# Kernel optimization log

Hardware: AMD Instinct MI355X
Metric: run time of the kernel (lower is better)

## Reference

```python
import jax, jax.numpy as jnp
import numpy as np

N_PHY = 12
NMUL = 4
WARM_UP = 365
NEARZERO = 1e-5
LENF = 15

# parameter_bounds order: BETA, FC, K0, K1, K2, LP, PERC, UZL, TT, CFMAX, CFR, CWH
PHY_LB = jnp.array([1.0, 50.0, 0.05, 0.01, 0.001, 0.2, 0.0, 0.0, -2.5, 0.5, 0.0, 0.0], dtype=jnp.float32)
PHY_UB = jnp.array([6.0, 1000.0, 0.9, 0.5, 0.2, 1.0, 10.0, 100.0, 2.5, 10.0, 0.1, 0.2], dtype=jnp.float32)
ROUTE_A_LB, ROUTE_A_UB = 0.0, 2.9
ROUTE_B_LB, ROUTE_B_UB = 0.0, 6.5


def _hbv_scan(p, t, pet, states, phy):
    """Run HBV step recurrence over time. p/t/pet: [T,G]; states: 5-tuple of [G,M]."""
    beta, fc, k0, k1, k2, lp, perc, uzl, tt, cfmax, cfr, cwh = phy  # each [G,M]

    def step(carry, xt):
        snowpack, meltwater, sm, suz, slz = carry
        Pt, Tt, PETt = xt
        Pt, Tt, PETt = Pt[:, None], Tt[:, None], PETt[:, None]  # [G,1] bcast vs [G,M]
        is_rain = (Tt >= tt).astype(sm.dtype)
        rain = Pt * is_rain
        snow = Pt * (1.0 - is_rain)
        snowpack = snowpack + snow
        melt = jnp.minimum(jnp.maximum(cfmax * (Tt - tt), 0.0), snowpack)
        meltwater = meltwater + melt
        snowpack = snowpack - melt
        refreeze = jnp.minimum(jnp.maximum(cfr * cfmax * (tt - Tt), 0.0), meltwater)
        snowpack = snowpack + refreeze
        meltwater = meltwater - refreeze
        tosoil = jnp.maximum(meltwater - cwh * snowpack, 0.0)
        meltwater = meltwater - tosoil
        soil_wetness = jnp.clip((sm / fc) ** beta, 0.0, 1.0)
        recharge = (rain + tosoil) * soil_wetness
        sm = sm + rain + tosoil - recharge
        excess = jnp.maximum(sm - fc, 0.0)
        sm = sm - excess
        evapfactor = jnp.clip(sm / (lp * fc), 0.0, 1.0)
        etact = jnp.minimum(sm, PETt * evapfactor)
        sm = jnp.maximum(sm - etact, NEARZERO)
        suz = suz + recharge + excess
        prc = jnp.minimum(suz, perc)
        suz = suz - prc
        q0 = k0 * jnp.maximum(suz - uzl, 0.0)
        suz = suz - q0
        q1 = k1 * suz
        suz = suz - q1
        slz = slz + prc
        q2 = k2 * slz
        slz = slz - q2
        return (snowpack, meltwater, sm, suz, slz), q0 + q1 + q2

    states, qs = jax.lax.scan(step, states, (p, t, pet))
    return qs, states  # qs: [T,G,M]


def _forward(x_phy, parameters):
    T, G, _ = x_phy.shape
    p, t, pet = x_phy[..., 0], x_phy[..., 1], x_phy[..., 2]
    # unpack physical params from last param timestep, map [0,1] -> bounds
    raw = parameters[-1, :, : N_PHY * NMUL].reshape(G, N_PHY, NMUL)
    phy_all = PHY_LB[None, :, None] + raw * (PHY_UB - PHY_LB)[None, :, None]
    phy = tuple(phy_all[:, i, :] for i in range(N_PHY))  # (beta, fc, k0, k1, k2, lp, perc, uzl, tt, cfmax, cfr, cwh)
    route = parameters[-1, :, N_PHY * NMUL :]
    a = ROUTE_A_LB + route[:, 0] * (ROUTE_A_UB - ROUTE_A_LB)
    b = ROUTE_B_LB + route[:, 1] * (ROUTE_B_UB - ROUTE_B_LB)

    s0 = jnp.full((G, NMUL), 0.001, dtype=x_phy.dtype)
    states = (s0, s0, s0, s0, s0)

    # warm-up under stop_gradient (matches torch.no_grad in original)
    phy_ng = jax.tree_util.tree_map(jax.lax.stop_gradient, phy)
    q_warm, states = _hbv_scan(
        jax.lax.stop_gradient(p[:WARM_UP]),
        jax.lax.stop_gradient(t[:WARM_UP]),
        jax.lax.stop_gradient(pet[:WARM_UP]),
        states, phy_ng)
    states = jax.tree_util.tree_map(jax.lax.stop_gradient, states)
    q_warm = jax.lax.stop_gradient(q_warm)

    q_pred, _ = _hbv_scan(p[WARM_UP:], t[WARM_UP:], pet[WARM_UP:], states, phy)
    qs = jnp.concatenate([q_warm, q_pred], axis=0).mean(-1)  # [T,G]

    # gamma unit hydrograph weights, [LENF, G]
    tg = (jnp.arange(LENF, dtype=qs.dtype) + 0.5)[:, None]
    aa = jax.nn.relu(a)[None, :] + 0.1
    th = jax.nn.relu(b)[None, :] + 0.5
    w = (tg ** (aa - 1.0)) * jnp.exp(-tg / th) / (jnp.exp(jax.scipy.special.gammaln(aa)) * th ** aa)
    w = w / w.sum(0)

    # causal depthwise (per-basin) convolution along time
    conv = jax.vmap(lambda q, u: jnp.convolve(q, u)[:T])(qs.T, w.T)  # [G,T]
    streamflow = conv.T[:, :, None]  # [T,G,1]
    return streamflow[WARM_UP:]


def setup_inputs() -> dict:
    key = jax.random.key(0)
    k1, k2, k3, k4 = jax.random.split(key, 4)
    T, G = 2000, 4000
    prcp = jax.random.uniform(k1, (T, G), dtype=jnp.float32) * 10.0   # mm/day
    tmean = jax.random.normal(k2, (T, G), dtype=jnp.float32) * 8.0    # degC
    pet = jax.random.uniform(k3, (T, G), dtype=jnp.float32) * 5.0     # mm/day
    x_phy = jnp.stack([prcp, tmean, pet], axis=-1)
    parameters = jax.random.uniform(k4, (1, G, N_PHY * NMUL + 2), dtype=jnp.float32)
    return {"x_phy": x_phy, "parameters": parameters}


def reference(x_phy, parameters):
    return _forward(x_phy, parameters)
```

## Files before the change

kernel.cpp:

```cpp
#include <hip/hip_runtime.h>

#define TT    2000
#define NG    4000
#define WARM  365
#define LENF  15
#define NPHY  12
#define BLK   60
#define PAIRS (BLK / 2)
#define SLOTW 64
#define SLOTD (BLK * SLOTW)
#define NBLK  34
#define ROWF  (3 * NG)

typedef const float __attribute__((address_space(1)))* gptr_t;
typedef float __attribute__((address_space(3)))* lptr_t;
typedef __attribute__((ext_vector_type(2))) float f32x2;

__device__ __forceinline__ float quad_sum(float x) {
    int a = __builtin_amdgcn_update_dpp(0, __float_as_int(x), 0xB1, 0xF, 0xF, true);
    float s = x + __int_as_float(a);
    int b = __builtin_amdgcn_update_dpp(0, __float_as_int(s), 0x4E, 0xF, 0xF, true);
    return s + __int_as_float(b);
}

#define WG_BARRIER() asm volatile("s_waitcnt lgkmcnt(0)\n\ts_barrier" ::: "memory")

__global__ __launch_bounds__(256, 1) void hbv_pipe_kernel(
    const float* __restrict__ xphy,
    const float* __restrict__ prm,
    float* __restrict__ out)
{
    __shared__ float s_stage[3 * SLOTD];
    __shared__ f32x2 s_rt [2 * PAIRS * 64];
    __shared__ f32x2 s_rex[2 * PAIRS * 64];
    __shared__ f32x2 s_q  [2 * PAIRS * 64];

    const int lane = threadIdx.x & 63;
    const int wid  = threadIdx.x >> 6;
    const int g0   = blockIdx.x * 16;
    const int cell = lane >> 2;
    const int g    = g0 + cell;
    const int m    = lane & 3;

    const float* pg = prm + (size_t)g * (NPHY * 4 + 2);

    const float lb[NPHY] = {1.0f, 50.0f, 0.05f, 0.01f, 0.001f, 0.2f, 0.0f, 0.0f, -2.5f, 0.5f, 0.0f, 0.0f};
    const float ub[NPHY] = {6.0f, 1000.0f, 0.9f, 0.5f, 0.2f, 1.0f, 10.0f, 100.0f, 2.5f, 10.0f, 0.1f, 0.2f};
    float ph[NPHY];
    #pragma unroll
    for (int i = 0; i < NPHY; ++i)
        ph[i] = lb[i] + pg[i * 4 + m] * (ub[i] - lb[i]);

    const float beta = ph[0], fc = ph[1], k0 = ph[2], k1 = ph[3], k2 = ph[4],
                lp = ph[5], perc = ph[6], uzl = ph[7], ttp = ph[8],
                cfmax = ph[9], cfr = ph[10], cwh = ph[11];
    const float rfc    = 1.0f / fc;
    const float rlpfc  = 1.0f / (lp * fc);
    const float cfrcf  = cfr * cfmax;
    const float blfc   = beta * __builtin_amdgcn_logf(rfc);
    const float onemk1 = 1.0f - k1;
    const float onemk2 = 1.0f - k2;

    const float aa  = fmaxf(pg[48] * 2.9f, 0.0f) + 0.1f;
    const float th  = fmaxf(pg[49] * 6.5f, 0.0f) + 0.5f;
    const float rth = 1.0f / th;
    const float LOG2E = 1.4426950408889634f;
    float w[LENF];
    float wsum = 0.0f;
    #pragma unroll
    for (int k = 0; k < LENF; ++k) {
        const float tg = (float)k + 0.5f;
        const float e = (aa - 1.0f) * __builtin_log2f(tg) - tg * rth * LOG2E;
        w[k] = __builtin_amdgcn_exp2f(e);
        wsum += w[k];
    }
    const float rw = 0.25f / wsum;
    #pragma unroll
    for (int k = 0; k < LENF; ++k) w[k] *= rw;

    float snowpack = 0.001f, meltwater = 0.001f;
    float sm = 0.001f;
    float suz = 0.001f, slz = 0.001f;
    float qh[BLK + LENF - 1];
    #pragma unroll
    for (int d = 0; d < BLK + LENF - 1; ++d) qh[d] = 0.0f;

    const int loffd = (lane < 48 ? lane : 47);
    const float* ga = xphy + (size_t)(wid * 15) * ROWF + g0 * 3 + loffd;

    {
        float* ldst = &s_stage[(wid * 15) * SLOTW];
        #pragma unroll
        for (int cc = 0; cc < 15; ++cc) {
            __builtin_amdgcn_global_load_lds((gptr_t)ga, (lptr_t)(ldst + cc * SLOTW), 4, 0, 0);
            ga += ROWF;
        }
        ga += 45 * ROWF;
    }
    asm volatile("s_waitcnt vmcnt(0)" ::: "memory");
    WG_BARRIER();

    for (int i = 0; i <= NBLK + 2; ++i) {
        if (i < NBLK - 1) {
            const int sl = (i + 1) % 3;
            float* ldst = &s_stage[sl * SLOTD + (wid * 15) * SLOTW];
            if (i + 1 == NBLK - 1) {
                #pragma unroll
                for (int cc = 0; cc < 15; ++cc) {
                    int t = (NBLK - 1) * BLK + wid * 15 + cc;
                    if (t > TT - 1) t = TT - 1;
                    const float* gsrc = xphy + (size_t)t * ROWF + g0 * 3 + loffd;
                    __builtin_amdgcn_global_load_lds((gptr_t)gsrc, (lptr_t)(ldst + cc * SLOTW), 4, 0, 0);
                }
            } else {
                const float* gp2 = ga;
                #pragma unroll
                for (int cc = 0; cc < 15; ++cc) {
                    __builtin_amdgcn_global_load_lds((gptr_t)gp2, (lptr_t)(ldst + cc * SLOTW), 4, 0, 0);
                    gp2 += ROWF;
                }
                ga = gp2 + 45 * ROWF;
            }
        }

        if (wid == 0) {
            if (i < NBLK) {
                const float* sb = &s_stage[(i % 3) * SLOTD + cell * 3];
                f32x2* rtw = &s_rt[(i & 1) * (PAIRS * 64) + lane];
                float rt_even = 0.0f;
                #pragma unroll
                for (int j = 0; j < BLK; ++j) {
                    const float Pt = sb[j * SLOTW];
                    const float Tm = sb[j * SLOTW + 1];
                    const float dT      = Tm - ttp;
                    const float rain    = (Tm >= ttp) ? Pt : 0.0f;
                    const float snow    = Pt - rain;
                    const float meltcap = cfmax * fmaxf(dT, 0.0f);
                    const float refcap  = cfrcf * fmaxf(-dT, 0.0f);
                    snowpack += snow;
                    const float melt = fminf(meltcap, snowpack);
                    meltwater += melt;
                    snowpack  -= melt;
                    const float refreeze = fminf(refcap, meltwater);
                    meltwater -= refreeze;
                    snowpack  += refreeze;
                    const float tosoil = fmaxf(fmaf(-cwh, snowpack, meltwater), 0.0f);
                    meltwater -= tosoil;
                    const float rt = rain + tosoil;
                    if ((j & 1) == 0) rt_even = rt;
                    else {
                        f32x2 pr; pr[0] = rt_even; pr[1] = rt;
                        rtw[(j >> 1) * 64] = pr;
                    }
                }
            }
        } else if (wid == 1) {
            const int b = i - 1;
            if (b >= 0 && b < NBLK) {
                const float* sb = &s_stage[(b % 3) * SLOTD + cell * 3 + 2];
                const f32x2* rtr = &s_rt[(b & 1) * (PAIRS * 64) + lane];
                f32x2* rexw = &s_rex[(b & 1) * (PAIRS * 64) + lane];
                f32x2 prt; prt[0] = 0.0f; prt[1] = 0.0f;
                float rex_even = 0.0f;
                #pragma unroll
                for (int j = 0; j < BLK; ++j) {
                    if ((j & 1) == 0) prt = rtr[(j >> 1) * 64];
                    const float rt = ((j & 1) == 0) ? prt[0] : prt[1];
                    const float ev = sb[j * SLOTW];
                    const float sw    = __builtin_amdgcn_exp2f(fmaf(beta, __builtin_amdgcn_logf(sm), blfc));
                    const float smprt = sm + rt;
                    const float sm1   = fmaf(-rt, sw, smprt);
                    const float sm2   = fminf(sm1, fc);
                    const float uf    = fmaxf(fmaf(-ev, rlpfc, 1.0f), 0.0f);
                    const float av    = sm2 * uf;
                    const float cv    = sm2 - ev;
                    sm = fmaxf(fmaxf(av, cv), 1e-5f);
                    const float rex = fmaf(rt, sw, sm1 - sm2);
                    if ((j & 1) == 0) rex_even = rex;
                    else {
                        f32x2 pr; pr[0] = rex_even; pr[1] = rex;
                        rexw[(j >> 1) * 64] = pr;
                    }
                }
            }
        } else if (wid == 2) {
            const int b = i - 2;
            if (b >= 0 && b < NBLK) {
                const f32x2* rexr = &s_rex[(b & 1) * (PAIRS * 64) + lane];
                f32x2* qw = &s_q[(b & 1) * (PAIRS * 64) + lane];
                f32x2 prx; prx[0] = 0.0f; prx[1] = 0.0f;
                float q_even = 0.0f;
                #pragma unroll
                for (int j = 0; j < BLK; ++j) {
                    if ((j & 1) == 0) prx = rexr[(j >> 1) * 64];
                    const float rex = ((j & 1) == 0) ? prx[0] : prx[1];
                    const float suz1 = suz + rex;
                    const float prc  = fminf(suz1, perc);
                    const float suzA = suz1 - prc;
                    const float tq   = fmaxf(suzA - uzl, 0.0f);
                    const float q0   = k0 * tq;
                    const float suzB = fmaf(-k0, tq, suzA);
                    const float q1   = k1 * suzB;
                    suz = suzB * onemk1;
                    const float slz1 = slz + prc;
                    const float q2   = k2 * slz1;
                    slz = slz1 * onemk2;
                    const float q = quad_sum(q0 + q1 + q2);
                    if ((j & 1) == 0) q_even = q;
                    else {
                        f32x2 pr; pr[0] = q_even; pr[1] = q;
                        qw[(j >> 1) * 64] = pr;
                    }
                }
            }
        } else {
            const int b = i - 3;
            if (b >= 0 && b < NBLK) {
                const int t0 = b * BLK;
                const f32x2* qr = &s_q[(b & 1) * (PAIRS * 64) + lane];
                #pragma unroll
                for (int jp = 0; jp < PAIRS; ++jp) {
                    const f32x2 qp = qr[jp * 64];
                    qh[LENF - 1 + 2 * jp]     = qp[0];
                    qh[LENF - 1 + 2 * jp + 1] = qp[1];
                }
                float ov[BLK / 4];
                #pragma unroll
                for (int k = 0; k < BLK / 4; ++k) ov[k] = 0.0f;
                #pragma unroll
                for (int j = 0; j < BLK; ++j) {
                    float o = w[0] * qh[LENF - 1 + j];
                    #pragma unroll
                    for (int k = 1; k < LENF; ++k)
                        o = fmaf(w[k], qh[LENF - 1 + j - k], o);
                    const bool sel = ((j & 3) == m);
                    ov[j >> 2] = sel ? o : ov[j >> 2];
                }
                #pragma unroll
                for (int d = 0; d < LENF - 1; ++d) qh[d] = qh[d + BLK];
                #pragma unroll
                for (int k = 0; k < BLK / 4; ++k) {
                    const int j = k * 4 + m;
                    const int t = t0 + j;
                    if (t >= WARM && t < TT)
                        out[(size_t)(t - WARM) * NG + g] = ov[k];
                }
            }
        }

        asm volatile("s_waitcnt vmcnt(0)" ::: "memory");
        WG_BARRIER();
    }
}

extern "C" void kernel_launch(void* const* d_in, const int* in_sizes, int n_in,
                              void* d_out, int out_size, void* d_ws, size_t ws_size,
                              hipStream_t stream) {
    const float* xphy = (const float*)d_in[0];
    const float* prm  = (const float*)d_in[1];
    float* out = (float*)d_out;

    hbv_pipe_kernel<<<NG / 16, 256, 0, stream>>>(xphy, prm, out);
}
```

Baseline: 126.8 us.

## Split convolution into separate parallel kernel, shorten recurrence pipeline to three waves

Removes the fourth pipeline wave that did the 15-tap unit-hydrograph convolution inside the sequential kernel. The routing wave now writes the per-basin mean flow to a workspace buffer, and a second fully parallel kernel computes the gamma weights and the convolution over (basin, 8-step time tile). This shortens the per-block critical path and pipeline depth of the recurrence kernel, and runs the convolution across many more threads. The cost is an extra global write and read of the full flow series and a second launch. The first kernel also stores q for warm-up timesteps that the reference never outputs.

```diff
diff --git a/kernel.cpp b/kernel.cpp
--- a/kernel.cpp
+++ b/kernel.cpp
@@ -6,10 +6,9 @@
 #define LENF  15
 #define NPHY  12
 #define BLK   60
-#define PAIRS (BLK / 2)
+#define NBLK  34
 #define SLOTW 64
-#define SLOTD (BLK * SLOTW)
-#define NBLK  34
+#define SLOT  (BLK * SLOTW)
 #define ROWF  (3 * NG)
 
 typedef const float __attribute__((address_space(1)))* gptr_t;
@@ -25,15 +24,14 @@
 
 #define WG_BARRIER() asm volatile("s_waitcnt lgkmcnt(0)\n\ts_barrier" ::: "memory")
 
-__global__ __launch_bounds__(256, 1) void hbv_pipe_kernel(
+__global__ __launch_bounds__(192, 1) void hbv_chain_kernel(
     const float* __restrict__ xphy,
     const float* __restrict__ prm,
-    float* __restrict__ out)
+    float* __restrict__ qm)
 {
-    __shared__ float s_stage[3 * SLOTD];
-    __shared__ f32x2 s_rt [2 * PAIRS * 64];
-    __shared__ f32x2 s_rex[2 * PAIRS * 64];
-    __shared__ f32x2 s_q  [2 * PAIRS * 64];
+    __shared__ float s_stage[3 * SLOT];
+    __shared__ f32x2 s_rt [2 * (BLK / 2) * 64];
+    __shared__ f32x2 s_rex[2 * (BLK / 2) * 64];
 
     const int lane = threadIdx.x & 63;
     const int wid  = threadIdx.x >> 6;
@@ -54,79 +52,40 @@
     const float beta = ph[0], fc = ph[1], k0 = ph[2], k1 = ph[3], k2 = ph[4],
                 lp = ph[5], perc = ph[6], uzl = ph[7], ttp = ph[8],
                 cfmax = ph[9], cfr = ph[10], cwh = ph[11];
-    const float rfc    = 1.0f / fc;
     const float rlpfc  = 1.0f / (lp * fc);
     const float cfrcf  = cfr * cfmax;
-    const float blfc   = beta * __builtin_amdgcn_logf(rfc);
+    const float blfc   = beta * __builtin_amdgcn_logf(1.0f / fc);
     const float onemk1 = 1.0f - k1;
     const float onemk2 = 1.0f - k2;
-
-    const float aa  = fmaxf(pg[48] * 2.9f, 0.0f) + 0.1f;
-    const float th  = fmaxf(pg[49] * 6.5f, 0.0f) + 0.5f;
-    const float rth = 1.0f / th;
-    const float LOG2E = 1.4426950408889634f;
-    float w[LENF];
-    float wsum = 0.0f;
-    #pragma unroll
-    for (int k = 0; k < LENF; ++k) {
-        const float tg = (float)k + 0.5f;
-        const float e = (aa - 1.0f) * __builtin_log2f(tg) - tg * rth * LOG2E;
-        w[k] = __builtin_amdgcn_exp2f(e);
-        wsum += w[k];
-    }
-    const float rw = 0.25f / wsum;
-    #pragma unroll
-    for (int k = 0; k < LENF; ++k) w[k] *= rw;
 
     float snowpack = 0.001f, meltwater = 0.001f;
     float sm = 0.001f;
     float suz = 0.001f, slz = 0.001f;
-    float qh[BLK + LENF - 1];
-    #pragma unroll
-    for (int d = 0; d < BLK + LENF - 1; ++d) qh[d] = 0.0f;
 
     const int loffd = (lane < 48 ? lane : 47);
-    const float* ga = xphy + (size_t)(wid * 15) * ROWF + g0 * 3 + loffd;
-
-    {
-        float* ldst = &s_stage[(wid * 15) * SLOTW];
+
+    auto stage_blk = [&](int b) {
+        const int tb = b * BLK + wid * 20;
+        float* ldst = &s_stage[(b % 3) * SLOT + (wid * 20) * SLOTW];
         #pragma unroll
-        for (int cc = 0; cc < 15; ++cc) {
-            __builtin_amdgcn_global_load_lds((gptr_t)ga, (lptr_t)(ldst + cc * SLOTW), 4, 0, 0);
-            ga += ROWF;
+        for (int c = 0; c < 20; ++c) {
+            int t = tb + c; t = (t < TT) ? t : (TT - 1);
+            const float* src = xphy + (size_t)t * ROWF + g0 * 3 + loffd;
+            __builtin_amdgcn_global_load_lds((gptr_t)src, (lptr_t)(ldst + c * SLOTW), 4, 0, 0);
         }
-        ga += 45 * ROWF;
-    }
+    };
+
+    stage_blk(0);
     asm volatile("s_waitcnt vmcnt(0)" ::: "memory");
     WG_BARRIER();
 
-    for (int i = 0; i <= NBLK + 2; ++i) {
-        if (i < NBLK - 1) {
-            const int sl = (i + 1) % 3;
-            float* ldst = &s_stage[sl * SLOTD + (wid * 15) * SLOTW];
-            if (i + 1 == NBLK - 1) {
-                #pragma unroll
-                for (int cc = 0; cc < 15; ++cc) {
-                    int t = (NBLK - 1) * BLK + wid * 15 + cc;
-                    if (t > TT - 1) t = TT - 1;
-                    const float* gsrc = xphy + (size_t)t * ROWF + g0 * 3 + loffd;
-                    __builtin_amdgcn_global_load_lds((gptr_t)gsrc, (lptr_t)(ldst + cc * SLOTW), 4, 0, 0);
-                }
-            } else {
-                const float* gp2 = ga;
-                #pragma unroll
-                for (int cc = 0; cc < 15; ++cc) {
-                    __builtin_amdgcn_global_load_lds((gptr_t)gp2, (lptr_t)(ldst + cc * SLOTW), 4, 0, 0);
-                    gp2 += ROWF;
-                }
-                ga = gp2 + 45 * ROWF;
-            }
-        }
+    for (int i = 0; i <= NBLK + 1; ++i) {
+        if (i < NBLK - 1) stage_blk(i + 1);
 
         if (wid == 0) {
             if (i < NBLK) {
-                const float* sb = &s_stage[(i % 3) * SLOTD + cell * 3];
-                f32x2* rtw = &s_rt[(i & 1) * (PAIRS * 64) + lane];
+                const float* sb = &s_stage[(i % 3) * SLOT + cell * 3];
+                f32x2* rtw = &s_rt[(i & 1) * ((BLK / 2) * 64) + lane];
                 float rt_even = 0.0f;
                 #pragma unroll
                 for (int j = 0; j < BLK; ++j) {
@@ -134,10 +93,10 @@
                     const float Tm = sb[j * SLOTW + 1];
                     const float dT      = Tm - ttp;
                     const float rain    = (Tm >= ttp) ? Pt : 0.0f;
-                    const float snow    = Pt - rain;
+                    const float snw     = Pt - rain;
                     const float meltcap = cfmax * fmaxf(dT, 0.0f);
                     const float refcap  = cfrcf * fmaxf(-dT, 0.0f);
-                    snowpack += snow;
+                    snowpack += snw;
                     const float melt = fminf(meltcap, snowpack);
                     meltwater += melt;
                     snowpack  -= melt;
@@ -148,52 +107,46 @@
                     meltwater -= tosoil;
                     const float rt = rain + tosoil;
                     if ((j & 1) == 0) rt_even = rt;
-                    else {
-                        f32x2 pr; pr[0] = rt_even; pr[1] = rt;
-                        rtw[(j >> 1) * 64] = pr;
-                    }
+                    else { f32x2 pr; pr[0] = rt_even; pr[1] = rt; rtw[(j >> 1) * 64] = pr; }
                 }
             }
         } else if (wid == 1) {
             const int b = i - 1;
             if (b >= 0 && b < NBLK) {
-                const float* sb = &s_stage[(b % 3) * SLOTD + cell * 3 + 2];
-                const f32x2* rtr = &s_rt[(b & 1) * (PAIRS * 64) + lane];
-                f32x2* rexw = &s_rex[(b & 1) * (PAIRS * 64) + lane];
-                f32x2 prt; prt[0] = 0.0f; prt[1] = 0.0f;
+                const float* sbe = &s_stage[(b % 3) * SLOT + cell * 3 + 2];
+                const f32x2* rtr = &s_rt[(b & 1) * ((BLK / 2) * 64) + lane];
+                f32x2* rexw = &s_rex[(b & 1) * ((BLK / 2) * 64) + lane];
+                f32x2 rp; rp[0] = 0.0f; rp[1] = 0.0f;
                 float rex_even = 0.0f;
                 #pragma unroll
                 for (int j = 0; j < BLK; ++j) {
-                    if ((j & 1) == 0) prt = rtr[(j >> 1) * 64];
-                    const float rt = ((j & 1) == 0) ? prt[0] : prt[1];
-                    const float ev = sb[j * SLOTW];
+                    if ((j & 1) == 0) rp = rtr[(j >> 1) * 64];
+                    const float rt = ((j & 1) == 0) ? rp[0] : rp[1];
+                    const float ev = sbe[j * SLOTW];
                     const float sw    = __builtin_amdgcn_exp2f(fmaf(beta, __builtin_amdgcn_logf(sm), blfc));
-                    const float smprt = sm + rt;
-                    const float sm1   = fmaf(-rt, sw, smprt);
+                    const float sp    = sm + rt;
+                    const float sm1   = fmaf(-rt, sw, sp);
                     const float sm2   = fminf(sm1, fc);
                     const float uf    = fmaxf(fmaf(-ev, rlpfc, 1.0f), 0.0f);
-                    const float av    = sm2 * uf;
-                    const float cv    = sm2 - ev;
-                    sm = fmaxf(fmaxf(av, cv), 1e-5f);
+                    sm = fmaxf(fmaxf(sm2 * uf, sm2 - ev), 1e-5f);
                     const float rex = fmaf(rt, sw, sm1 - sm2);
                     if ((j & 1) == 0) rex_even = rex;
-                    else {
-                        f32x2 pr; pr[0] = rex_even; pr[1] = rex;
-                        rexw[(j >> 1) * 64] = pr;
-                    }
+                    else { f32x2 pr; pr[0] = rex_even; pr[1] = rex; rexw[(j >> 1) * 64] = pr; }
                 }
             }
-        } else if (wid == 2) {
+        } else {
             const int b = i - 2;
             if (b >= 0 && b < NBLK) {
-                const f32x2* rexr = &s_rex[(b & 1) * (PAIRS * 64) + lane];
-                f32x2* qw = &s_q[(b & 1) * (PAIRS * 64) + lane];
-                f32x2 prx; prx[0] = 0.0f; prx[1] = 0.0f;
-                float q_even = 0.0f;
+                const int t0 = b * BLK;
+                const f32x2* rexr = &s_rex[(b & 1) * ((BLK / 2) * 64) + lane];
+                f32x2 rp; rp[0] = 0.0f; rp[1] = 0.0f;
+                float ov[BLK / 4];
+                #pragma unroll
+                for (int k = 0; k < BLK / 4; ++k) ov[k] = 0.0f;
                 #pragma unroll
                 for (int j = 0; j < BLK; ++j) {
-                    if ((j & 1) == 0) prx = rexr[(j >> 1) * 64];
-                    const float rex = ((j & 1) == 0) ? prx[0] : prx[1];
+                    if ((j & 1) == 0) rp = rexr[(j >> 1) * 64];
+                    const float rex = ((j & 1) == 0) ? rp[0] : rp[1];
                     const float suz1 = suz + rex;
                     const float prc  = fminf(suz1, perc);
                     const float suzA = suz1 - prc;
@@ -202,54 +155,72 @@
                     const float suzB = fmaf(-k0, tq, suzA);
                     const float q1   = k1 * suzB;
                     suz = suzB * onemk1;
-                    const float slz1 = slz + prc;
-                    const float q2   = k2 * slz1;
-                    slz = slz1 * onemk2;
+                    const float sl1  = slz + prc;
+                    const float q2   = k2 * sl1;
+                    slz = sl1 * onemk2;
                     const float q = quad_sum(q0 + q1 + q2);
-                    if ((j & 1) == 0) q_even = q;
-                    else {
-                        f32x2 pr; pr[0] = q_even; pr[1] = q;
-                        qw[(j >> 1) * 64] = pr;
-                    }
-                }
-            }
-        } else {
-            const int b = i - 3;
-            if (b >= 0 && b < NBLK) {
-                const int t0 = b * BLK;
-                const f32x2* qr = &s_q[(b & 1) * (PAIRS * 64) + lane];
-                #pragma unroll
-                for (int jp = 0; jp < PAIRS; ++jp) {
-                    const f32x2 qp = qr[jp * 64];
-                    qh[LENF - 1 + 2 * jp]     = qp[0];
-                    qh[LENF - 1 + 2 * jp + 1] = qp[1];
-                }
-                float ov[BLK / 4];
-                #pragma unroll
-                for (int k = 0; k < BLK / 4; ++k) ov[k] = 0.0f;
-                #pragma unroll
-                for (int j = 0; j < BLK; ++j) {
-                    float o = w[0] * qh[LENF - 1 + j];
-                    #pragma unroll
-                    for (int k = 1; k < LENF; ++k)
-                        o = fmaf(w[k], qh[LENF - 1 + j - k], o);
                     const bool sel = ((j & 3) == m);
-                    ov[j >> 2] = sel ? o : ov[j >> 2];
-                }
-                #pragma unroll
-                for (int d = 0; d < LENF - 1; ++d) qh[d] = qh[d + BLK];
+                    ov[j >> 2] = sel ? q : ov[j >> 2];
+                }
                 #pragma unroll
                 for (int k = 0; k < BLK / 4; ++k) {
-                    const int j = k * 4 + m;
-                    const int t = t0 + j;
-                    if (t >= WARM && t < TT)
-                        out[(size_t)(t - WARM) * NG + g] = ov[k];
+                    const int t = t0 + k * 4 + m;
+                    if (t < TT) qm[(size_t)t * NG + g] = ov[k];
                 }
             }
         }
 
         asm volatile("s_waitcnt vmcnt(0)" ::: "memory");
         WG_BARRIER();
+    }
+}
+
+__global__ __launch_bounds__(256) void hbv_conv_kernel(
+    const float* __restrict__ qm,
+    const float* __restrict__ prm,
+    float* __restrict__ out)
+{
+    const int g = blockIdx.x * 256 + threadIdx.x;
+    if (g >= NG) return;
+    const int t0 = WARM + blockIdx.y * 8;
+
+    const float* pr = prm + (size_t)g * 50;
+    const float aa  = fmaxf(pr[48] * 2.9f, 0.0f) + 0.1f;
+    const float th  = fmaxf(pr[49] * 6.5f, 0.0f) + 0.5f;
+    const float aam1 = aa - 1.0f;
+    const float rthl = 1.4426950408889634f / th;
+
+    const float L2TG[LENF] = {
+        -1.0f, 0.5849625007211562f, 1.3219280948873623f, 1.8073549220576042f,
+        2.169925001442312f, 2.4594316186372973f, 2.700439718141092f,
+        2.9068905956085187f, 3.087462841250339f, 3.247927513443585f,
+        3.3923174227787602f, 3.523561956057013f, 3.643856189774724f,
+        3.754887502163468f, 3.857980995127572f };
+
+    float w[LENF];
+    float wsum = 0.0f;
+    #pragma unroll
+    for (int k = 0; k < LENF; ++k) {
+        const float tg = (float)k + 0.5f;
+        w[k] = __builtin_amdgcn_exp2f(fmaf(aam1, L2TG[k], -tg * rthl));
+        wsum += w[k];
+    }
+    const float rw = 0.25f / wsum;
+
+    float qv[22];
+    #pragma unroll
+    for (int j = 0; j < 22; ++j) {
+        int t = t0 - 14 + j; t = (t < TT) ? t : (TT - 1);
+        qv[j] = qm[(size_t)t * NG + g];
+    }
+    #pragma unroll
+    for (int c = 0; c < 8; ++c) {
+        float o = 0.0f;
+        #pragma unroll
+        for (int k = 0; k < LENF; ++k)
+            o = fmaf(w[k], qv[14 + c - k], o);
+        const int t = t0 + c;
+        if (t < TT) out[(size_t)(t - WARM) * NG + g] = o * rw;
     }
 }
 
@@ -259,6 +230,10 @@
     const float* xphy = (const float*)d_in[0];
     const float* prm  = (const float*)d_in[1];
     float* out = (float*)d_out;
-
-    hbv_pipe_kernel<<<NG / 16, 256, 0, stream>>>(xphy, prm, out);
-}
+    float* qm  = (float*)d_ws;
+
+    hbv_chain_kernel<<<NG / 16, 192, 0, stream>>>(xphy, prm, qm);
+
+    dim3 grid2((NG + 255) / 256, (TT - WARM + 7) / 8);
+    hbv_conv_kernel<<<grid2, 256, 0, stream>>>(qm, prm, out);
+}
```

Result: slower. 142.9 us (+12.8%).

## Double-buffer staging, forward PET via stage-0 LDS, widen inter-stage LDS to float4

Applied to the files above, without the earlier changes.

Shrinks the input staging buffer from triple to double buffering and has wave 0 read PET along with P and T, passing it to wave 1 packed with rain+tosoil in float4 records. The rex and q handoffs between pipeline stages are widened from float2 to float4 LDS accesses, which halves the number of LDS transactions. The vmcnt wait moves inside each wave's branch, and the prefetch is simplified into a lambda that clamps the time index. Each staged block must now be consumed within one iteration, and wave 0 does extra LDS traffic for PET.

```diff
diff --git a/kernel.cpp b/kernel.cpp
--- a/kernel.cpp
+++ b/kernel.cpp
@@ -6,15 +6,14 @@
 #define LENF  15
 #define NPHY  12
 #define BLK   60
-#define PAIRS (BLK / 2)
+#define NBLK  34
 #define SLOTW 64
-#define SLOTD (BLK * SLOTW)
-#define NBLK  34
+#define SLOT  (BLK * SLOTW)
 #define ROWF  (3 * NG)
 
 typedef const float __attribute__((address_space(1)))* gptr_t;
 typedef float __attribute__((address_space(3)))* lptr_t;
-typedef __attribute__((ext_vector_type(2))) float f32x2;
+typedef __attribute__((ext_vector_type(4))) float f32x4;
 
 __device__ __forceinline__ float quad_sum(float x) {
     int a = __builtin_amdgcn_update_dpp(0, __float_as_int(x), 0xB1, 0xF, 0xF, true);
@@ -30,10 +29,10 @@
     const float* __restrict__ prm,
     float* __restrict__ out)
 {
-    __shared__ float s_stage[3 * SLOTD];
-    __shared__ f32x2 s_rt [2 * PAIRS * 64];
-    __shared__ f32x2 s_rex[2 * PAIRS * 64];
-    __shared__ f32x2 s_q  [2 * PAIRS * 64];
+    __shared__ float s_stage[2 * SLOT];
+    __shared__ f32x4 s_rtev[2 * (BLK / 2) * 64];
+    __shared__ f32x4 s_rex [2 * (BLK / 4) * 64];
+    __shared__ f32x4 s_q   [2 * (BLK / 4) * 64];
 
     const int lane = threadIdx.x & 63;
     const int wid  = threadIdx.x >> 6;
@@ -54,10 +53,9 @@
     const float beta = ph[0], fc = ph[1], k0 = ph[2], k1 = ph[3], k2 = ph[4],
                 lp = ph[5], perc = ph[6], uzl = ph[7], ttp = ph[8],
                 cfmax = ph[9], cfr = ph[10], cwh = ph[11];
-    const float rfc    = 1.0f / fc;
     const float rlpfc  = 1.0f / (lp * fc);
     const float cfrcf  = cfr * cfmax;
-    const float blfc   = beta * __builtin_amdgcn_logf(rfc);
+    const float blfc   = beta * __builtin_amdgcn_logf(1.0f / fc);
     const float onemk1 = 1.0f - k1;
     const float onemk2 = 1.0f - k2;
 
@@ -86,58 +84,41 @@
     for (int d = 0; d < BLK + LENF - 1; ++d) qh[d] = 0.0f;
 
     const int loffd = (lane < 48 ? lane : 47);
-    const float* ga = xphy + (size_t)(wid * 15) * ROWF + g0 * 3 + loffd;
-
-    {
-        float* ldst = &s_stage[(wid * 15) * SLOTW];
+
+    auto stage_blk = [&](int b) {
+        const int tb = b * BLK + wid * 15;
+        float* ldst = &s_stage[(b & 1) * SLOT + (wid * 15) * SLOTW];
         #pragma unroll
-        for (int cc = 0; cc < 15; ++cc) {
-            __builtin_amdgcn_global_load_lds((gptr_t)ga, (lptr_t)(ldst + cc * SLOTW), 4, 0, 0);
-            ga += ROWF;
+        for (int c = 0; c < 15; ++c) {
+            int t = tb + c; t = (t < TT) ? t : (TT - 1);
+            const float* src = xphy + (size_t)t * ROWF + g0 * 3 + loffd;
+            __builtin_amdgcn_global_load_lds((gptr_t)src, (lptr_t)(ldst + c * SLOTW), 4, 0, 0);
         }
-        ga += 45 * ROWF;
-    }
+    };
+
+    stage_blk(0);
     asm volatile("s_waitcnt vmcnt(0)" ::: "memory");
     WG_BARRIER();
 
     for (int i = 0; i <= NBLK + 2; ++i) {
-        if (i < NBLK - 1) {
-            const int sl = (i + 1) % 3;
-            float* ldst = &s_stage[sl * SLOTD + (wid * 15) * SLOTW];
-            if (i + 1 == NBLK - 1) {
-                #pragma unroll
-                for (int cc = 0; cc < 15; ++cc) {
-                    int t = (NBLK - 1) * BLK + wid * 15 + cc;
-                    if (t > TT - 1) t = TT - 1;
-                    const float* gsrc = xphy + (size_t)t * ROWF + g0 * 3 + loffd;
-                    __builtin_amdgcn_global_load_lds((gptr_t)gsrc, (lptr_t)(ldst + cc * SLOTW), 4, 0, 0);
-                }
-            } else {
-                const float* gp2 = ga;
-                #pragma unroll
-                for (int cc = 0; cc < 15; ++cc) {
-                    __builtin_amdgcn_global_load_lds((gptr_t)gp2, (lptr_t)(ldst + cc * SLOTW), 4, 0, 0);
-                    gp2 += ROWF;
-                }
-                ga = gp2 + 45 * ROWF;
-            }
-        }
+        if (i + 1 < NBLK) stage_blk(i + 1);
 
         if (wid == 0) {
             if (i < NBLK) {
-                const float* sb = &s_stage[(i % 3) * SLOTD + cell * 3];
-                f32x2* rtw = &s_rt[(i & 1) * (PAIRS * 64) + lane];
-                float rt_even = 0.0f;
+                const float* sb = &s_stage[(i & 1) * SLOT + cell * 3];
+                f32x4* rtw = &s_rtev[(i & 1) * ((BLK / 2) * 64) + lane];
+                float rtE = 0.0f, evE = 0.0f;
                 #pragma unroll
                 for (int j = 0; j < BLK; ++j) {
                     const float Pt = sb[j * SLOTW];
                     const float Tm = sb[j * SLOTW + 1];
+                    const float ev = sb[j * SLOTW + 2];
                     const float dT      = Tm - ttp;
                     const float rain    = (Tm >= ttp) ? Pt : 0.0f;
-                    const float snow    = Pt - rain;
+                    const float snw     = Pt - rain;
                     const float meltcap = cfmax * fmaxf(dT, 0.0f);
                     const float refcap  = cfrcf * fmaxf(-dT, 0.0f);
-                    snowpack += snow;
+                    snowpack += snw;
                     const float melt = fminf(meltcap, snowpack);
                     meltwater += melt;
                     snowpack  -= melt;
@@ -147,53 +128,55 @@
                     const float tosoil = fmaxf(fmaf(-cwh, snowpack, meltwater), 0.0f);
                     meltwater -= tosoil;
                     const float rt = rain + tosoil;
-                    if ((j & 1) == 0) rt_even = rt;
+                    if ((j & 1) == 0) { rtE = rt; evE = ev; }
                     else {
-                        f32x2 pr; pr[0] = rt_even; pr[1] = rt;
-                        rtw[(j >> 1) * 64] = pr;
+                        f32x4 q; q[0] = rtE; q[1] = evE; q[2] = rt; q[3] = ev;
+                        rtw[(j >> 1) * 64] = q;
                     }
                 }
             }
+            asm volatile("s_waitcnt vmcnt(0)" ::: "memory");
         } else if (wid == 1) {
             const int b = i - 1;
             if (b >= 0 && b < NBLK) {
-                const float* sb = &s_stage[(b % 3) * SLOTD + cell * 3 + 2];
-                const f32x2* rtr = &s_rt[(b & 1) * (PAIRS * 64) + lane];
-                f32x2* rexw = &s_rex[(b & 1) * (PAIRS * 64) + lane];
-                f32x2 prt; prt[0] = 0.0f; prt[1] = 0.0f;
-                float rex_even = 0.0f;
-                #pragma unroll
-                for (int j = 0; j < BLK; ++j) {
-                    if ((j & 1) == 0) prt = rtr[(j >> 1) * 64];
-                    const float rt = ((j & 1) == 0) ? prt[0] : prt[1];
-                    const float ev = sb[j * SLOTW];
-                    const float sw    = __builtin_amdgcn_exp2f(fmaf(beta, __builtin_amdgcn_logf(sm), blfc));
-                    const float smprt = sm + rt;
-                    const float sm1   = fmaf(-rt, sw, smprt);
-                    const float sm2   = fminf(sm1, fc);
-                    const float uf    = fmaxf(fmaf(-ev, rlpfc, 1.0f), 0.0f);
-                    const float av    = sm2 * uf;
-                    const float cv    = sm2 - ev;
-                    sm = fmaxf(fmaxf(av, cv), 1e-5f);
+                const f32x4* rtr = &s_rtev[(b & 1) * ((BLK / 2) * 64) + lane];
+                f32x4* rexw = &s_rex[(b & 1) * ((BLK / 4) * 64) + lane];
+                f32x4 rp; rp[0] = 0.0f; rp[1] = 0.0f; rp[2] = 0.0f; rp[3] = 0.0f;
+                float x0 = 0.0f, x1 = 0.0f, x2 = 0.0f;
+                #pragma unroll
+                for (int j = 0; j < BLK; ++j) {
+                    if ((j & 1) == 0) rp = rtr[(j >> 1) * 64];
+                    const float rt = ((j & 1) == 0) ? rp[0] : rp[2];
+                    const float ev = ((j & 1) == 0) ? rp[1] : rp[3];
+                    const float sw  = __builtin_amdgcn_exp2f(fmaf(beta, __builtin_amdgcn_logf(sm), blfc));
+                    const float sp  = sm + rt;
+                    const float sm1 = fmaf(-rt, sw, sp);
+                    const float sm2 = fminf(sm1, fc);
+                    const float uf  = fmaxf(fmaf(-ev, rlpfc, 1.0f), 0.0f);
+                    sm = fmaxf(fmaxf(sm2 * uf, sm2 - ev), 1e-5f);
                     const float rex = fmaf(rt, sw, sm1 - sm2);
-                    if ((j & 1) == 0) rex_even = rex;
+                    if ((j & 3) == 0)      x0 = rex;
+                    else if ((j & 3) == 1) x1 = rex;
+                    else if ((j & 3) == 2) x2 = rex;
                     else {
-                        f32x2 pr; pr[0] = rex_even; pr[1] = rex;
-                        rexw[(j >> 1) * 64] = pr;
+                        f32x4 q; q[0] = x0; q[1] = x1; q[2] = x2; q[3] = rex;
+                        rexw[(j >> 2) * 64] = q;
                     }
                 }
             }
+            asm volatile("s_waitcnt vmcnt(0)" ::: "memory");
         } else if (wid == 2) {
             const int b = i - 2;
             if (b >= 0 && b < NBLK) {
-                const f32x2* rexr = &s_rex[(b & 1) * (PAIRS * 64) + lane];
-                f32x2* qw = &s_q[(b & 1) * (PAIRS * 64) + lane];
-                f32x2 prx; prx[0] = 0.0f; prx[1] = 0.0f;
-                float q_even = 0.0f;
-                #pragma unroll
-                for (int j = 0; j < BLK; ++j) {
-                    if ((j & 1) == 0) prx = rexr[(j >> 1) * 64];
-                    const float rex = ((j & 1) == 0) ? prx[0] : prx[1];
+                const f32x4* rexr = &s_rex[(b & 1) * ((BLK / 4) * 64) + lane];
+                f32x4* qw = &s_q[(b & 1) * ((BLK / 4) * 64) + lane];
+                f32x4 rp; rp[0] = 0.0f; rp[1] = 0.0f; rp[2] = 0.0f; rp[3] = 0.0f;
+                float q0v = 0.0f, q1v = 0.0f, q2v = 0.0f;
+                #pragma unroll
+                for (int j = 0; j < BLK; ++j) {
+                    if ((j & 3) == 0) rp = rexr[(j >> 2) * 64];
+                    const float rex = ((j & 3) == 0) ? rp[0] : ((j & 3) == 1) ? rp[1]
+                                     : ((j & 3) == 2) ? rp[2] : rp[3];
                     const float suz1 = suz + rex;
                     const float prc  = fminf(suz1, perc);
                     const float suzA = suz1 - prc;
@@ -202,27 +185,32 @@
                     const float suzB = fmaf(-k0, tq, suzA);
                     const float q1   = k1 * suzB;
                     suz = suzB * onemk1;
-                    const float slz1 = slz + prc;
-                    const float q2   = k2 * slz1;
-                    slz = slz1 * onemk2;
+                    const float sl1  = slz + prc;
+                    const float q2   = k2 * sl1;
+                    slz = sl1 * onemk2;
                     const float q = quad_sum(q0 + q1 + q2);
-                    if ((j & 1) == 0) q_even = q;
+                    if ((j & 3) == 0)      q0v = q;
+                    else if ((j & 3) == 1) q1v = q;
+                    else if ((j & 3) == 2) q2v = q;
                     else {
-                        f32x2 pr; pr[0] = q_even; pr[1] = q;
-                        qw[(j >> 1) * 64] = pr;
+                        f32x4 qq; qq[0] = q0v; qq[1] = q1v; qq[2] = q2v; qq[3] = q;
+                        qw[(j >> 2) * 64] = qq;
                     }
                 }
             }
+            asm volatile("s_waitcnt vmcnt(0)" ::: "memory");
         } else {
             const int b = i - 3;
             if (b >= 0 && b < NBLK) {
                 const int t0 = b * BLK;
-                const f32x2* qr = &s_q[(b & 1) * (PAIRS * 64) + lane];
-                #pragma unroll
-                for (int jp = 0; jp < PAIRS; ++jp) {
-                    const f32x2 qp = qr[jp * 64];
-                    qh[LENF - 1 + 2 * jp]     = qp[0];
-                    qh[LENF - 1 + 2 * jp + 1] = qp[1];
+                const f32x4* qr = &s_q[(b & 1) * ((BLK / 4) * 64) + lane];
+                #pragma unroll
+                for (int p = 0; p < BLK / 4; ++p) {
+                    const f32x4 qq = qr[p * 64];
+                    qh[LENF - 1 + 4 * p]     = qq[0];
+                    qh[LENF - 1 + 4 * p + 1] = qq[1];
+                    qh[LENF - 1 + 4 * p + 2] = qq[2];
+                    qh[LENF - 1 + 4 * p + 3] = qq[3];
                 }
                 float ov[BLK / 4];
                 #pragma unroll
@@ -246,9 +234,9 @@
                         out[(size_t)(t - WARM) * NG + g] = ov[k];
                 }
             }
+            asm volatile("s_waitcnt vmcnt(0)" ::: "memory");
         }
 
-        asm volatile("s_waitcnt vmcnt(0)" ::: "memory");
         WG_BARRIER();
     }
 }
```

After: 146.7 us. 15.7% more time.
